# Optimization experiments

Measured on AMD Instinct MI355X. Metric: run time of the kernel, lower is better.

The kernel has to match this reference:

```python
import jax, jax.numpy as jnp
import numpy as np

N_DATA = 131072
N_HID = 32768
D = 256
E1 = 524288  # data -> hidden
E2 = 524288  # hidden -> hidden
E3 = 524288  # hidden -> data


def setup_inputs() -> dict:
    key = jax.random.key(0)
    ks = jax.random.split(key, 32)
    rn = lambda k, shape, s=0.05: (jax.random.normal(k, shape, jnp.float32) * s)
    inp = {
        "data_x": jax.random.normal(ks[0], (N_DATA, 8), jnp.float32),
        "hidden_x": jax.random.normal(ks[1], (N_HID, 3), jnp.float32),
        "dh_src": jax.random.randint(ks[2], (E1,), 0, N_DATA, jnp.int32),
        "dh_dst": jax.random.randint(ks[3], (E1,), 0, N_HID, jnp.int32),
        "hh_src": jax.random.randint(ks[4], (E2,), 0, N_HID, jnp.int32),
        "hh_dst": jax.random.randint(ks[5], (E2,), 0, N_HID, jnp.int32),
        "hd_src": jax.random.randint(ks[6], (E3,), 0, N_HID, jnp.int32),
        "hd_dst": jax.random.randint(ks[7], (E3,), 0, N_DATA, jnp.int32),
        # encoder params
        "enc_src_w": rn(ks[8], (D, 8)), "enc_src_b": rn(ks[9], (D,)),
        "enc_dst_w": rn(ks[10], (D, 3)), "enc_dst_b": rn(ks[11], (D,)),
        "enc_wl": rn(ks[12], (D, D)), "enc_bl": rn(ks[13], (D,)), "enc_wr": rn(ks[14], (D, D)),
        # processor params
        "proc_wl": rn(ks[15], (D, D)), "proc_bl": rn(ks[16], (D,)), "proc_wr": rn(ks[17], (D, D)),
        "proc_mlp_w": rn(ks[18], (D, D)), "proc_mlp_b": rn(ks[19], (D,)),
        # decoder params
        "dec_src_w": rn(ks[20], (D, D)), "dec_src_b": rn(ks[21], (D,)),
        "dec_dst_w": rn(ks[22], (D, 8)), "dec_dst_b": rn(ks[23], (D,)),
        "dec_wl": rn(ks[24], (D, D)), "dec_bl": rn(ks[25], (D,)), "dec_wr": rn(ks[26], (D, D)),
        "out_w": rn(ks[27], (8, D)), "out_b": rn(ks[28], (8,)),
    }
    return inp


def _gelu(x):
    return jax.nn.gelu(x, approximate=False)  # torch nn.GELU default (erf)


def _sage(x_src, x_dst, src, dst, wl, bl, wr, n_dst):
    """PyG SAGEConv, mean aggregation: lin_l(mean_j x_src[j]) + lin_r(x_dst)."""
    msg = x_src[src]                                              # [E, D] gather
    agg = jax.ops.segment_sum(msg, dst, num_segments=n_dst)       # [n_dst, D]
    cnt = jax.ops.segment_sum(jnp.ones((src.shape[0], 1), msg.dtype), dst,
                              num_segments=n_dst)
    mean = agg / jnp.maximum(cnt, 1.0)
    return mean @ wl.T + bl + x_dst @ wr.T


def reference(data_x, hidden_x, dh_src, dh_dst, hh_src, hh_dst, hd_src, hd_dst,
              enc_src_w, enc_src_b, enc_dst_w, enc_dst_b, enc_wl, enc_bl, enc_wr,
              proc_wl, proc_bl, proc_wr, proc_mlp_w, proc_mlp_b,
              dec_src_w, dec_src_b, dec_dst_w, dec_dst_b, dec_wl, dec_bl, dec_wr,
              out_w, out_b):
    # ---- encoder: data -> hidden ----
    h_data = _gelu(data_x @ enc_src_w.T + enc_src_b)
    h_hid = _gelu(hidden_x @ enc_dst_w.T + enc_dst_b)
    h_hid = _gelu(_sage(h_data, h_hid, dh_src, dh_dst, enc_wl, enc_bl, enc_wr, N_HID))
    # ---- processor: hidden -> hidden, then GELU-Linear-GELU MLP ----
    h_hid = _sage(h_hid, h_hid, hh_src, hh_dst, proc_wl, proc_bl, proc_wr, N_HID)
    h_hid = _gelu(_gelu(h_hid) @ proc_mlp_w.T + proc_mlp_b)
    # ---- decoder: hidden -> data ----
    s = _gelu(h_hid @ dec_src_w.T + dec_src_b)
    d = _gelu(data_x @ dec_dst_w.T + dec_dst_b)
    d = _gelu(_sage(s, d, hd_src, hd_dst, dec_wl, dec_bl, dec_wr, N_DATA))
    return d @ out_w.T + out_b  # [N_DATA, 8]
```

## Files before the change

kernel.cpp:

```cpp
#include <hip/hip_runtime.h>
#include <stdint.h>

#define NDATA 131072
#define NHID  32768
#define NEDGE 524288

typedef __bf16 bf16_t;
typedef __bf16 bf16x4 __attribute__((ext_vector_type(4)));
typedef __bf16 bf16x8 __attribute__((ext_vector_type(8)));
typedef float  f32x4  __attribute__((ext_vector_type(4)));

__device__ __forceinline__ float gelu_f(float x) {
    return 0.5f * x * (1.0f + erff(x * 0.7071067811865476f));
}

__device__ __forceinline__ void glds16(const void* g, void* l) {
    auto* gp = reinterpret_cast<const __attribute__((address_space(1))) uint32_t*>(
        reinterpret_cast<uintptr_t>(g));
    auto* lp = reinterpret_cast<__attribute__((address_space(3))) uint32_t*>(
        reinterpret_cast<uintptr_t>(l));
    __builtin_amdgcn_global_load_lds(gp, lp, 16, 0, 0);
}

struct WPtrs { const float* p[9]; };

__global__ __launch_bounds__(256)
void cvt_w_kernel(WPtrs wp, bf16_t* __restrict__ out) {
    const int i = blockIdx.x * 256 + threadIdx.x;
    if (i < 8 * 65536) {
        const int wsel = i >> 16, off = i & 65535;
        out[i] = (bf16_t)wp.p[wsel][off];
    } else {
        out[i] = (bf16_t)wp.p[8][i - 8 * 65536];
    }
}

struct EdgePtrs { const int* src[3]; const int* dst[3]; };

__device__ __forceinline__ int cnt_off_of(int g) { return g == 0 ? 0 : (g == 1 ? NHID : 2 * NHID); }
__device__ __forceinline__ int rp_off_of(int g)  { return g == 0 ? 0 : (g == 1 ? NHID + 1 : 2 * NHID + 2); }
__device__ __forceinline__ int shift_of(int g)   { return g == 2 ? 10 : 8; }

__global__ __launch_bounds__(256)
void hist3(EdgePtrs ep, int* __restrict__ cnt_all) {
    const int g = blockIdx.x >> 11;
    const int i = ((blockIdx.x & 2047) << 8) + threadIdx.x;
    atomicAdd(&cnt_all[cnt_off_of(g) + ep.dst[g][i]], 1);
}

__global__ __launch_bounds__(256)
void scan_blk3(const int* __restrict__ cnt_all, int* __restrict__ pre_all,
               int* __restrict__ blk) {
    __shared__ int sh[256];
    const int bid = blockIdx.x;
    int g, local;
    if (bid < 32)      { g = 0; local = bid; }
    else if (bid < 64) { g = 1; local = bid - 32; }
    else               { g = 2; local = bid - 64; }
    const int t = threadIdx.x;
    const int cbase = cnt_off_of(g) + local * 1024 + t * 4;
    const int pbase = rp_off_of(g)  + local * 1024 + t * 4;
    int4 v = *(const int4*)(cnt_all + cbase);
    sh[t] = v.x + v.y + v.z + v.w;
    __syncthreads();
    for (int off = 1; off < 256; off <<= 1) {
        int other = 0;
        if (t >= off) other = sh[t - off];
        __syncthreads();
        if (t >= off) sh[t] += other;
        __syncthreads();
    }
    const int excl = (t == 0) ? 0 : sh[t - 1];
    int4 o;
    o.x = excl; o.y = o.x + v.x; o.z = o.y + v.y; o.w = o.z + v.z;
    *(int4*)(pre_all + pbase) = o;
    if (t == 255) blk[bid] = sh[255];
}

__global__ __launch_bounds__(256)
void scan_add3(const int* __restrict__ pre_all, const int* __restrict__ blk,
               int* __restrict__ rp_all, int* __restrict__ binA) {
    __shared__ int sh[256];
    const int bid = blockIdx.x;
    int g, local, gbase;
    if (bid < 32)      { g = 0; local = bid;      gbase = 0; }
    else if (bid < 64) { g = 1; local = bid - 32; gbase = 32; }
    else               { g = 2; local = bid - 64; gbase = 64; }
    const int t = threadIdx.x;
    int part = 0;
    if (t < local) part = blk[gbase + t];
    sh[t] = part;
    __syncthreads();
    for (int o2 = 128; o2 > 0; o2 >>= 1) {
        if (t < o2) sh[t] += sh[t + o2];
        __syncthreads();
    }
    const int off = sh[0];
    const int idx = local * 1024 + t * 4;
    const int pbase = rp_off_of(g) + idx;
    int4 v = *(const int4*)(pre_all + pbase);
    v.x += off; v.y += off; v.z += off; v.w += off;
    *(int4*)(rp_all + pbase) = v;
    const int bw = 1 << shift_of(g);
    if ((idx & (bw - 1)) == 0) binA[g * 128 + (idx >> shift_of(g))] = v.x;
    if (local == 0 && t == 0) {
        const int n = (g == 2) ? NDATA : NHID;
        rp_all[rp_off_of(g) + n] = NEDGE;
    }
}

__global__ __launch_bounds__(256)
void partition3(EdgePtrs ep, int* __restrict__ binA, int2* __restrict__ pairs) {
    __shared__ int hist[128], base[128], cur[128];
    const int g = blockIdx.x >> 7;
    const int blk = blockIdx.x & 127;
    const int t = threadIdx.x;
    const int shift = shift_of(g);
    const int e_base = blk * 4096;
    const int* src = ep.src[g];
    const int* dst = ep.dst[g];
    if (t < 128) { hist[t] = 0; cur[t] = 0; }
    __syncthreads();
    #pragma unroll
    for (int it = 0; it < 16; ++it) {
        const int d = dst[e_base + it * 256 + t];
        atomicAdd(&hist[d >> shift], 1);
    }
    __syncthreads();
    if (t < 128) base[t] = atomicAdd(&binA[g * 128 + t], hist[t]);
    __syncthreads();
    #pragma unroll
    for (int it = 0; it < 16; ++it) {
        const int e = e_base + it * 256 + t;
        const int s = src[e], d = dst[e];
        const int b = d >> shift;
        const int l = atomicAdd(&cur[b], 1);
        pairs[(size_t)g * NEDGE + base[b] + l] = make_int2(s, d);
    }
}

__global__ __launch_bounds__(256)
void binsort3(const int2* __restrict__ pairs, const int* __restrict__ rp_all,
              int* __restrict__ sorted_all) {
    __shared__ int cur[1024];
    const int g = blockIdx.x >> 7;
    const int b = blockIdx.x & 127;
    const int t = threadIdx.x;
    const int shift = shift_of(g);
    const int W = 1 << shift;
    const int d0 = b << shift;
    const int rpo = rp_off_of(g);
    for (int i = t; i < W; i += 256) cur[i] = rp_all[rpo + d0 + i];
    __syncthreads();
    const int e0 = rp_all[rpo + d0];
    const int e1 = rp_all[rpo + d0 + W];
    for (int e = e0 + t; e < e1; e += 256) {
        const int2 p = pairs[(size_t)g * NEDGE + e];
        const int pos = atomicAdd(&cur[p.y - d0], 1);
        sorted_all[(size_t)g * NEDGE + pos] = p.x;
    }
}

__global__ __launch_bounds__(256)
void csr_gather_mean(const bf16_t* __restrict__ feat, const int* __restrict__ row_ptr,
                     const int* __restrict__ sorted_src, bf16_t* __restrict__ mean, int n) {
    const int lane = threadIdx.x & 63;
    const int half = lane >> 5;
    const int col8 = (lane & 31) * 8;
    const int w = blockIdx.x * 4 + (threadIdx.x >> 6);
    if (w >= n) return;
    const int e0 = row_ptr[w], e1 = row_ptr[w + 1];
    float acc[8] = {0.f, 0.f, 0.f, 0.f, 0.f, 0.f, 0.f, 0.f};
    int e = e0 + half;
    for (; e + 2 < e1; e += 4) {
        const int s0 = sorted_src[e], s1 = sorted_src[e + 2];
        const bf16x8 v0 = *(const bf16x8*)(feat + (size_t)s0 * 256 + col8);
        const bf16x8 v1 = *(const bf16x8*)(feat + (size_t)s1 * 256 + col8);
        #pragma unroll
        for (int j = 0; j < 8; ++j) acc[j] += (float)v0[j] + (float)v1[j];
    }
    for (; e < e1; e += 2) {
        const int s0 = sorted_src[e];
        const bf16x8 v0 = *(const bf16x8*)(feat + (size_t)s0 * 256 + col8);
        #pragma unroll
        for (int j = 0; j < 8; ++j) acc[j] += (float)v0[j];
    }
    #pragma unroll
    for (int j = 0; j < 8; ++j) acc[j] += __shfl_xor(acc[j], 32, 64);
    if (half == 0) {
        const float ic = 1.0f / fmaxf((float)(e1 - e0), 1.0f);
        bf16x8 r;
        #pragma unroll
        for (int j = 0; j < 8; ++j) r[j] = (bf16_t)(acc[j] * ic);
        *(bf16x8*)(mean + (size_t)w * 256 + col8) = r;
    }
}

__global__ __launch_bounds__(256)
void enc_both(const float* __restrict__ hx, const float* __restrict__ w3,
              const float* __restrict__ b3, bf16_t* __restrict__ out3,
              const float* __restrict__ dx, const float* __restrict__ w8,
              const float* __restrict__ b8, bf16_t* __restrict__ out8) {
    __shared__ float ws[8 * 256];
    __shared__ float bs[256];
    const int t = threadIdx.x;
    const bool is8 = (blockIdx.x >= 512);
    if (is8) {
        #pragma unroll
        for (int j = 0; j < 8; ++j) ws[j * 256 + t] = w8[t * 8 + j];
        bs[t] = b8[t];
    } else {
        #pragma unroll
        for (int j = 0; j < 3; ++j) ws[j * 256 + t] = w3[t * 3 + j];
        bs[t] = b3[t];
    }
    __syncthreads();
    const int lane = t & 63, wv = t >> 6;
    const int f0 = lane * 4;
    const float4 b4 = *(const float4*)(&bs[f0]);
    if (!is8) {
        for (int node = blockIdx.x * 4 + wv; node < NHID; node += 512 * 4) {
            const float* xr = hx + (size_t)node * 3;
            float xv[3];
            #pragma unroll
            for (int j = 0; j < 3; ++j) xv[j] = xr[j];
            float a0 = b4.x, a1 = b4.y, a2 = b4.z, a3 = b4.w;
            #pragma unroll
            for (int j = 0; j < 3; ++j) {
                const float4 w4 = *(const float4*)(&ws[j * 256 + f0]);
                a0 += xv[j] * w4.x; a1 += xv[j] * w4.y;
                a2 += xv[j] * w4.z; a3 += xv[j] * w4.w;
            }
            bf16x4 r;
            r[0] = (bf16_t)gelu_f(a0); r[1] = (bf16_t)gelu_f(a1);
            r[2] = (bf16_t)gelu_f(a2); r[3] = (bf16_t)gelu_f(a3);
            *(bf16x4*)(out3 + (size_t)node * 256 + f0) = r;
        }
    } else {
        for (int node = (blockIdx.x - 512) * 4 + wv; node < NDATA; node += 2048 * 4) {
            const float* xr = dx + (size_t)node * 8;
            float xv[8];
            #pragma unroll
            for (int j = 0; j < 8; ++j) xv[j] = xr[j];
            float a0 = b4.x, a1 = b4.y, a2 = b4.z, a3 = b4.w;
            #pragma unroll
            for (int j = 0; j < 8; ++j) {
                const float4 w4 = *(const float4*)(&ws[j * 256 + f0]);
                a0 += xv[j] * w4.x; a1 += xv[j] * w4.y;
                a2 += xv[j] * w4.z; a3 += xv[j] * w4.w;
            }
            bf16x4 r;
            r[0] = (bf16_t)gelu_f(a0); r[1] = (bf16_t)gelu_f(a1);
            r[2] = (bf16_t)gelu_f(a2); r[3] = (bf16_t)gelu_f(a3);
            *(bf16x4*)(out8 + (size_t)node * 256 + f0) = r;
        }
    }
}

template<int DUAL>
__global__ __launch_bounds__(256)
void mfma_gemm(const bf16_t* __restrict__ A1, const bf16_t* __restrict__ W1,
               const bf16_t* __restrict__ A2, const bf16_t* __restrict__ W2,
               const float* __restrict__ bias, bf16_t* __restrict__ C) {
    __shared__ bf16_t As[4 * 64 * 8];
    __shared__ bf16_t Bs[4 * 128 * 8];
    const int t = threadIdx.x;
    const int w = t >> 6, lane = t & 63;
    const int l15 = lane & 15, l4 = lane >> 4;
    const int m0 = (blockIdx.x >> 1) * 64;
    const int n0 = (blockIdx.x & 1) * 128;

    f32x4 acc[4][2];
    #pragma unroll
    for (int nb = 0; nb < 2; ++nb) {
        const float bv = bias[n0 + w * 32 + nb * 16 + l15];
        #pragma unroll
        for (int m = 0; m < 4; ++m) {
            acc[m][nb][0] = bv; acc[m][nb][1] = bv; acc[m][nb][2] = bv; acc[m][nb][3] = bv;
        }
    }

    #pragma unroll
    for (int p = 0; p <= DUAL; ++p) {
        const bf16_t* Ap = p ? A2 : A1;
        const bf16_t* Wp = p ? W2 : W1;
        for (int kt = 0; kt < 8; ++kt) {
            const int k0 = kt * 32;
            __syncthreads();
            glds16(Ap + (size_t)(m0 + lane) * 256 + k0 + w * 8, &As[(w * 64) * 8]);
            glds16(Wp + (size_t)(n0 + lane) * 256 + k0 + w * 8, &Bs[(w * 128) * 8]);
            glds16(Wp + (size_t)(n0 + 64 + lane) * 256 + k0 + w * 8, &Bs[(w * 128 + 64) * 8]);
            __syncthreads();
            bf16x8 af[4], bfr[2];
            #pragma unroll
            for (int m = 0; m < 4; ++m)
                af[m] = *(const bf16x8*)(&As[(l4 * 64 + m * 16 + l15) * 8]);
            #pragma unroll
            for (int nb = 0; nb < 2; ++nb)
                bfr[nb] = *(const bf16x8*)(&Bs[(l4 * 128 + w * 32 + nb * 16 + l15) * 8]);
            #pragma unroll
            for (int m = 0; m < 4; ++m)
                #pragma unroll
                for (int nb = 0; nb < 2; ++nb)
                    acc[m][nb] = __builtin_amdgcn_mfma_f32_16x16x32_bf16(af[m], bfr[nb], acc[m][nb], 0, 0, 0);
        }
    }

    #pragma unroll
    for (int m = 0; m < 4; ++m) {
        #pragma unroll
        for (int nb = 0; nb < 2; ++nb) {
            const int col = n0 + w * 32 + nb * 16 + l15;
            #pragma unroll
            for (int i = 0; i < 4; ++i) {
                const int row = m0 + m * 16 + l4 * 4 + i;
                C[(size_t)row * 256 + col] = (bf16_t)gelu_f(acc[m][nb][i]);
            }
        }
    }
}

__global__ __launch_bounds__(256)
void dec_gemm(const bf16_t* __restrict__ A1, const bf16_t* __restrict__ W1,
              const float* __restrict__ xdat, const float* __restrict__ Wd,
              const float* __restrict__ bd, const bf16_t* __restrict__ W2,
              const float* __restrict__ bias, const bf16_t* __restrict__ owb,
              const float* __restrict__ ob, float* __restrict__ out) {
    __shared__ __align__(16) char smem[25600];
    bf16_t* As   = (bf16_t*)smem;
    bf16_t* Bs   = (bf16_t*)(smem + 4096);
    bf16_t* wd16 = (bf16_t*)(smem + 20480);
    float*  bdS  = (float*)(smem + 24576);
    bf16_t* tt   = (bf16_t*)smem;
    float*  part = (float*)(smem + 16384);

    const int t = threadIdx.x;
    const int w = t >> 6, lane = t & 63;
    const int l15 = lane & 15, l4 = lane >> 4;
    const int m0 = blockIdx.x * 64;

    {
        const float4 wa = *(const float4*)(Wd + t * 8);
        const float4 wb = *(const float4*)(Wd + t * 8 + 4);
        bf16x8 wv;
        wv[0] = (bf16_t)wa.x; wv[1] = (bf16_t)wa.y; wv[2] = (bf16_t)wa.z; wv[3] = (bf16_t)wa.w;
        wv[4] = (bf16_t)wb.x; wv[5] = (bf16_t)wb.y; wv[6] = (bf16_t)wb.z; wv[7] = (bf16_t)wb.w;
        *(bf16x8*)(&wd16[t * 8]) = wv;
        bdS[t] = bd[t];
    }
    bf16x8 af_x;
    #pragma unroll
    for (int j = 0; j < 8; ++j) af_x[j] = (bf16_t)0.0f;
    if (l4 == 0) {
        const float* xrp = xdat + (size_t)(m0 + w * 16 + l15) * 8;
        const float4 xa = *(const float4*)(xrp);
        const float4 xb = *(const float4*)(xrp + 4);
        af_x[0] = (bf16_t)xa.x; af_x[1] = (bf16_t)xa.y; af_x[2] = (bf16_t)xa.z; af_x[3] = (bf16_t)xa.w;
        af_x[4] = (bf16_t)xb.x; af_x[5] = (bf16_t)xb.y; af_x[6] = (bf16_t)xb.z; af_x[7] = (bf16_t)xb.w;
    }

    f32x4 acc[4][4];
    #pragma unroll
    for (int nb = 0; nb < 4; ++nb) {
        const float bv = bias[w * 64 + nb * 16 + l15];
        #pragma unroll
        for (int m = 0; m < 4; ++m) {
            acc[m][nb][0] = bv; acc[m][nb][1] = bv; acc[m][nb][2] = bv; acc[m][nb][3] = bv;
        }
    }
    __syncthreads();

    #pragma unroll
    for (int p = 0; p < 2; ++p) {
        const bf16_t* Wp = p ? W2 : W1;
        for (int kt = 0; kt < 8; ++kt) {
            const int k0 = kt * 32;
            __syncthreads();
            if (p == 0) {
                glds16(A1 + (size_t)(m0 + lane) * 256 + k0 + w * 8, &As[(w * 64) * 8]);
            } else {
                #pragma unroll
                for (int nb2 = 0; nb2 < 2; ++nb2) {
                    const int cl = nb2 * 16 + l15;
                    const int col = k0 + cl;
                    f32x4 ad;
                    const float bv = bdS[col];
                    ad[0] = bv; ad[1] = bv; ad[2] = bv; ad[3] = bv;
                    bf16x8 bf_d;
                    #pragma unroll
                    for (int j = 0; j < 8; ++j) bf_d[j] = (bf16_t)0.0f;
                    if (l4 == 0) bf_d = *(const bf16x8*)(&wd16[col * 8]);
                    ad = __builtin_amdgcn_mfma_f32_16x16x32_bf16(af_x, bf_d, ad, 0, 0, 0);
                    const int kq = cl >> 3, jj = cl & 7;
                    #pragma unroll
                    for (int i = 0; i < 4; ++i)
                        As[(kq * 64 + w * 16 + l4 * 4 + i) * 8 + jj] = (bf16_t)gelu_f(ad[i]);
                }
            }
            #pragma unroll
            for (int q = 0; q < 4; ++q)
                glds16(Wp + (size_t)(w * 64 + lane) * 256 + k0 + q * 8,
                       &Bs[(q * 256 + w * 64) * 8]);
            __syncthreads();
            bf16x8 af[4], bfr[4];
            #pragma unroll
            for (int m = 0; m < 4; ++m)
                af[m] = *(const bf16x8*)(&As[(l4 * 64 + m * 16 + l15) * 8]);
            #pragma unroll
            for (int nb = 0; nb < 4; ++nb)
                bfr[nb] = *(const bf16x8*)(&Bs[(l4 * 256 + w * 64 + nb * 16 + l15) * 8]);
            #pragma unroll
            for (int m = 0; m < 4; ++m)
                #pragma unroll
                for (int nb = 0; nb < 4; ++nb)
                    acc[m][nb] = __builtin_amdgcn_mfma_f32_16x16x32_bf16(af[m], bfr[nb], acc[m][nb], 0, 0, 0);
        }
    }

    __syncthreads();

    bf16x8 owf[2];
    #pragma unroll
    for (int s = 0; s < 2; ++s) {
        #pragma unroll
        for (int j = 0; j < 8; ++j) owf[s][j] = (bf16_t)0.0f;
        if (l15 < 8)
            owf[s] = *(const bf16x8*)(owb + l15 * 256 + w * 64 + s * 32 + l4 * 8);
    }

    bf16_t* ttw = tt + w * 2048;
    #pragma unroll
    for (int h = 0; h < 2; ++h) {
        #pragma unroll
        for (int mm = 0; mm < 2; ++mm) {
            const int m = h * 2 + mm;
            #pragma unroll
            for (int nb = 0; nb < 4; ++nb) {
                const int col = nb * 16 + l15;
                const int kg = col >> 3, cj = col & 7;
                #pragma unroll
                for (int i = 0; i < 4; ++i) {
                    const int rl = mm * 16 + l4 * 4 + i;
                    ttw[(kg * 32 + rl) * 8 + cj] = (bf16_t)gelu_f(acc[m][nb][i]);
                }
            }
        }
        f32x4 accp[2];
        #pragma unroll
        for (int mb = 0; mb < 2; ++mb) {
            accp[mb][0] = 0.f; accp[mb][1] = 0.f; accp[mb][2] = 0.f; accp[mb][3] = 0.f;
            #pragma unroll
            for (int s = 0; s < 2; ++s) {
                const bf16x8 af = *(const bf16x8*)(&ttw[((s * 4 + l4) * 32 + mb * 16 + l15) * 8]);
                accp[mb] = __builtin_amdgcn_mfma_f32_16x16x32_bf16(af, owf[s], accp[mb], 0, 0, 0);
            }
        }
        __syncthreads();
        #pragma unroll
        for (int mb = 0; mb < 2; ++mb)
            #pragma unroll
            for (int i = 0; i < 4; ++i)
                part[(w * 32 + mb * 16 + l4 * 4 + i) * 16 + l15] = accp[mb][i];
        __syncthreads();
        {
            const int row = t >> 3, o = t & 7;
            const float v = part[(0 * 32 + row) * 16 + o] + part[(1 * 32 + row) * 16 + o]
                          + part[(2 * 32 + row) * 16 + o] + part[(3 * 32 + row) * 16 + o] + ob[o];
            out[(size_t)(m0 + h * 32 + row) * 8 + o] = v;
        }
    }
}


extern "C" void kernel_launch(void* const* d_in, const int* in_sizes, int n_in,
                              void* d_out, int out_size, void* d_ws, size_t ws_size,
                              hipStream_t stream) {
    const float* data_x   = (const float*)d_in[0];
    const float* hidden_x = (const float*)d_in[1];
    const int* dh_src = (const int*)d_in[2];
    const int* dh_dst = (const int*)d_in[3];
    const int* hh_src = (const int*)d_in[4];
    const int* hh_dst = (const int*)d_in[5];
    const int* hd_src = (const int*)d_in[6];
    const int* hd_dst = (const int*)d_in[7];
    const float* enc_src_w = (const float*)d_in[8];
    const float* enc_src_b = (const float*)d_in[9];
    const float* enc_dst_w = (const float*)d_in[10];
    const float* enc_dst_b = (const float*)d_in[11];
    const float* enc_wl = (const float*)d_in[12];
    const float* enc_bl = (const float*)d_in[13];
    const float* enc_wr = (const float*)d_in[14];
    const float* proc_wl = (const float*)d_in[15];
    const float* proc_bl = (const float*)d_in[16];
    const float* proc_wr = (const float*)d_in[17];
    const float* proc_mlp_w = (const float*)d_in[18];
    const float* proc_mlp_b = (const float*)d_in[19];
    const float* dec_src_w = (const float*)d_in[20];
    const float* dec_src_b = (const float*)d_in[21];
    const float* dec_dst_w = (const float*)d_in[22];
    const float* dec_dst_b = (const float*)d_in[23];
    const float* dec_wl = (const float*)d_in[24];
    const float* dec_bl = (const float*)d_in[25];
    const float* dec_wr = (const float*)d_in[26];
    const float* out_w  = (const float*)d_in[27];
    const float* out_b  = (const float*)d_in[28];
    float* out = (float*)d_out;

    bf16_t* h_a   = (bf16_t*)d_ws;
    bf16_t* h_b   = h_a + (size_t)NHID * 256;
    bf16_t* h_c   = h_b + (size_t)NHID * 256;
    bf16_t* h_msg = h_c + (size_t)NHID * 256;
    bf16_t* dmean = h_msg + (size_t)NDATA * 256;
    bf16_t* wbuf  = dmean + (size_t)NDATA * 256;
    int* cnt_all    = (int*)(wbuf + 8 * 65536 + 2048);
    int* rp_all     = cnt_all + (2 * NHID + NDATA);
    int* sorted_all = rp_all + (2 * NHID + NDATA + 3);
    int* blk_sums   = sorted_all + (size_t)3 * NEDGE;
    int* binA       = blk_sums + 192;
    int2* pairs     = (int2*)(((uintptr_t)(binA + 384) + 15) & ~(uintptr_t)15);

    bf16_t* W_enc_wl  = wbuf + 0 * 65536;
    bf16_t* W_enc_wr  = wbuf + 1 * 65536;
    bf16_t* W_proc_wl = wbuf + 2 * 65536;
    bf16_t* W_proc_wr = wbuf + 3 * 65536;
    bf16_t* W_mlp     = wbuf + 4 * 65536;
    bf16_t* W_dec_src = wbuf + 5 * 65536;
    bf16_t* W_dec_wl  = wbuf + 6 * 65536;
    bf16_t* W_dec_wr  = wbuf + 7 * 65536;
    bf16_t* W_out     = wbuf + 8 * 65536;

    const int* rp_dh = rp_all;
    const int* rp_hh = rp_all + NHID + 1;
    const int* rp_hd = rp_all + 2 * NHID + 2;
    const int* so_dh = sorted_all;
    const int* so_hh = sorted_all + NEDGE;
    const int* so_hd = sorted_all + 2 * (size_t)NEDGE;

    WPtrs wp;
    wp.p[0] = enc_wl;  wp.p[1] = enc_wr;  wp.p[2] = proc_wl; wp.p[3] = proc_wr;
    wp.p[4] = proc_mlp_w; wp.p[5] = dec_src_w; wp.p[6] = dec_wl; wp.p[7] = dec_wr;
    wp.p[8] = out_w;
    cvt_w_kernel<<<2056, 256, 0, stream>>>(wp, wbuf);

    EdgePtrs ep;
    ep.src[0] = dh_src; ep.dst[0] = dh_dst;
    ep.src[1] = hh_src; ep.dst[1] = hh_dst;
    ep.src[2] = hd_src; ep.dst[2] = hd_dst;
    hipMemsetAsync(cnt_all, 0, (size_t)(2 * NHID + NDATA) * sizeof(int), stream);
    hist3<<<3 * 2048, 256, 0, stream>>>(ep, cnt_all);
    scan_blk3<<<192, 256, 0, stream>>>(cnt_all, rp_all, blk_sums);
    scan_add3<<<192, 256, 0, stream>>>(rp_all, blk_sums, rp_all, binA);
    partition3<<<3 * 128, 256, 0, stream>>>(ep, binA, pairs);
    binsort3<<<3 * 128, 256, 0, stream>>>(pairs, rp_all, sorted_all);

    enc_both<<<2560, 256, 0, stream>>>(hidden_x, enc_dst_w, enc_dst_b, h_a,
                                       data_x, enc_src_w, enc_src_b, h_msg);
    csr_gather_mean<<<NHID / 4, 256, 0, stream>>>(h_msg, rp_dh, so_dh, h_b, NHID);
    mfma_gemm<1><<<(NHID / 64) * 2, 256, 0, stream>>>(h_b, W_enc_wl, h_a, W_enc_wr, enc_bl, h_c);

    csr_gather_mean<<<NHID / 4, 256, 0, stream>>>(h_c, rp_hh, so_hh, h_a, NHID);
    mfma_gemm<1><<<(NHID / 64) * 2, 256, 0, stream>>>(h_a, W_proc_wl, h_c, W_proc_wr, proc_bl, h_b);
    mfma_gemm<0><<<(NHID / 64) * 2, 256, 0, stream>>>(h_b, W_mlp, nullptr, nullptr, proc_mlp_b, h_a);
    mfma_gemm<0><<<(NHID / 64) * 2, 256, 0, stream>>>(h_a, W_dec_src, nullptr, nullptr, dec_src_b, h_b);

    csr_gather_mean<<<NDATA / 4, 256, 0, stream>>>(h_b, rp_hd, so_hd, dmean, NDATA);
    dec_gemm<<<NDATA / 64, 256, 0, stream>>>(dmean, W_dec_wl, data_x, dec_dst_w, dec_dst_b,
                                             W_dec_wr, dec_bl, W_out, out_b, out);
}
```

Baseline: 466.1 us.

## Fuse CSR gather-mean into SAGE GEMM kernels via LDS-resident mean tiles

Removes the standalone csr_gather_mean launches. Each GEMM block now gathers and averages the neighbor features for its 64 rows directly into shared memory, then runs the lin_l MFMA pass from LDS and the lin_r pass with A read directly from global memory. This drops the write and re-read of the mean buffers, which matters most for the large decoder buffer, and saves three launches. In exchange, blocks become 64x256 tiles with much larger LDS footprints, halving the grid for the hidden-node GEMMs. The latency-bound gather may then run with lower occupancy, and each wave serializes its 16 rows.

```diff
diff --git a/kernel.cpp b/kernel.cpp
--- a/kernel.cpp
+++ b/kernel.cpp
@@ -20,6 +20,11 @@
     auto* lp = reinterpret_cast<__attribute__((address_space(3))) uint32_t*>(
         reinterpret_cast<uintptr_t>(l));
     __builtin_amdgcn_global_load_lds(gp, lp, 16, 0, 0);
+}
+
+__device__ __forceinline__ void vm_fence0() {
+    asm volatile("s_waitcnt vmcnt(0)" ::: "memory");
+    __builtin_amdgcn_sched_barrier(0);
 }
 
 struct WPtrs { const float* p[9]; };
@@ -162,41 +167,6 @@
 }
 
 __global__ __launch_bounds__(256)
-void csr_gather_mean(const bf16_t* __restrict__ feat, const int* __restrict__ row_ptr,
-                     const int* __restrict__ sorted_src, bf16_t* __restrict__ mean, int n) {
-    const int lane = threadIdx.x & 63;
-    const int half = lane >> 5;
-    const int col8 = (lane & 31) * 8;
-    const int w = blockIdx.x * 4 + (threadIdx.x >> 6);
-    if (w >= n) return;
-    const int e0 = row_ptr[w], e1 = row_ptr[w + 1];
-    float acc[8] = {0.f, 0.f, 0.f, 0.f, 0.f, 0.f, 0.f, 0.f};
-    int e = e0 + half;
-    for (; e + 2 < e1; e += 4) {
-        const int s0 = sorted_src[e], s1 = sorted_src[e + 2];
-        const bf16x8 v0 = *(const bf16x8*)(feat + (size_t)s0 * 256 + col8);
-        const bf16x8 v1 = *(const bf16x8*)(feat + (size_t)s1 * 256 + col8);
-        #pragma unroll
-        for (int j = 0; j < 8; ++j) acc[j] += (float)v0[j] + (float)v1[j];
-    }
-    for (; e < e1; e += 2) {
-        const int s0 = sorted_src[e];
-        const bf16x8 v0 = *(const bf16x8*)(feat + (size_t)s0 * 256 + col8);
-        #pragma unroll
-        for (int j = 0; j < 8; ++j) acc[j] += (float)v0[j];
-    }
-    #pragma unroll
-    for (int j = 0; j < 8; ++j) acc[j] += __shfl_xor(acc[j], 32, 64);
-    if (half == 0) {
-        const float ic = 1.0f / fmaxf((float)(e1 - e0), 1.0f);
-        bf16x8 r;
-        #pragma unroll
-        for (int j = 0; j < 8; ++j) r[j] = (bf16_t)(acc[j] * ic);
-        *(bf16x8*)(mean + (size_t)w * 256 + col8) = r;
-    }
-}
-
-__global__ __launch_bounds__(256)
 void enc_both(const float* __restrict__ hx, const float* __restrict__ w3,
               const float* __restrict__ b3, bf16_t* __restrict__ out3,
               const float* __restrict__ dx, const float* __restrict__ w8,
@@ -257,11 +227,128 @@
     }
 }
 
-template<int DUAL>
-__global__ __launch_bounds__(256)
-void mfma_gemm(const bf16_t* __restrict__ A1, const bf16_t* __restrict__ W1,
-               const bf16_t* __restrict__ A2, const bf16_t* __restrict__ W2,
-               const float* __restrict__ bias, bf16_t* __restrict__ C) {
+__device__ __forceinline__ void gather_tile(const bf16_t* __restrict__ feat,
+                                            const int* __restrict__ rp,
+                                            const int* __restrict__ ss,
+                                            bf16_t* __restrict__ Asg,
+                                            int m0, int w, int lane) {
+    const int half = lane >> 5;
+    const int kq = lane & 31;
+    const int colb = kq * 8;
+    for (int rr = 0; rr < 16; ++rr) {
+        const int row = w * 16 + rr;
+        const int g0 = rp[m0 + row], g1 = rp[m0 + row + 1];
+        float a8[8] = {0.f, 0.f, 0.f, 0.f, 0.f, 0.f, 0.f, 0.f};
+        int e = g0 + half;
+        for (; e + 2 < g1; e += 4) {
+            const int s0 = ss[e], s1 = ss[e + 2];
+            const bf16x8 v0 = *(const bf16x8*)(feat + (size_t)s0 * 256 + colb);
+            const bf16x8 v1 = *(const bf16x8*)(feat + (size_t)s1 * 256 + colb);
+            #pragma unroll
+            for (int j = 0; j < 8; ++j) a8[j] += (float)v0[j] + (float)v1[j];
+        }
+        for (; e < g1; e += 2) {
+            const int s0 = ss[e];
+            const bf16x8 v0 = *(const bf16x8*)(feat + (size_t)s0 * 256 + colb);
+            #pragma unroll
+            for (int j = 0; j < 8; ++j) a8[j] += (float)v0[j];
+        }
+        #pragma unroll
+        for (int j = 0; j < 8; ++j) a8[j] += __shfl_xor(a8[j], 32, 64);
+        if (half == 0) {
+            const float ic = 1.0f / fmaxf((float)(g1 - g0), 1.0f);
+            bf16x8 r;
+            #pragma unroll
+            for (int j = 0; j < 8; ++j) r[j] = (bf16_t)(a8[j] * ic);
+            *(bf16x8*)(&Asg[(kq * 64 + row) * 8]) = r;
+        }
+    }
+}
+
+__global__ __launch_bounds__(256)
+void gemm_gather(const bf16_t* __restrict__ feat, const int* __restrict__ rp,
+                 const int* __restrict__ ss, const bf16_t* __restrict__ W1,
+                 const bf16_t* __restrict__ A2, const bf16_t* __restrict__ W2,
+                 const float* __restrict__ bias, bf16_t* __restrict__ C) {
+    __shared__ bf16_t Asg[32 * 64 * 8];
+    __shared__ bf16_t Bs[4 * 256 * 8];
+    const int t = threadIdx.x;
+    const int w = t >> 6, lane = t & 63;
+    const int l15 = lane & 15, l4 = lane >> 4;
+    const int m0 = blockIdx.x * 64;
+
+    gather_tile(feat, rp, ss, Asg, m0, w, lane);
+
+    f32x4 acc[4][4];
+    #pragma unroll
+    for (int nb = 0; nb < 4; ++nb) {
+        const float bv = bias[w * 64 + nb * 16 + l15];
+        #pragma unroll
+        for (int m = 0; m < 4; ++m) {
+            acc[m][nb][0] = bv; acc[m][nb][1] = bv; acc[m][nb][2] = bv; acc[m][nb][3] = bv;
+        }
+    }
+    __syncthreads();
+
+    for (int kt = 0; kt < 8; ++kt) {
+        const int k0 = kt * 32;
+        #pragma unroll
+        for (int q = 0; q < 4; ++q)
+            glds16(W1 + (size_t)(w * 64 + lane) * 256 + k0 + q * 8,
+                   &Bs[(q * 256 + w * 64) * 8]);
+        vm_fence0();
+        bf16x8 af[4], bfr[4];
+        #pragma unroll
+        for (int m = 0; m < 4; ++m)
+            af[m] = *(const bf16x8*)(&Asg[((kt * 4 + l4) * 64 + m * 16 + l15) * 8]);
+        #pragma unroll
+        for (int nb = 0; nb < 4; ++nb)
+            bfr[nb] = *(const bf16x8*)(&Bs[(l4 * 256 + w * 64 + nb * 16 + l15) * 8]);
+        #pragma unroll
+        for (int m = 0; m < 4; ++m)
+            #pragma unroll
+            for (int nb = 0; nb < 4; ++nb)
+                acc[m][nb] = __builtin_amdgcn_mfma_f32_16x16x32_bf16(af[m], bfr[nb], acc[m][nb], 0, 0, 0);
+    }
+    for (int kt = 0; kt < 8; ++kt) {
+        const int k0 = kt * 32;
+        #pragma unroll
+        for (int q = 0; q < 4; ++q)
+            glds16(W2 + (size_t)(w * 64 + lane) * 256 + k0 + q * 8,
+                   &Bs[(q * 256 + w * 64) * 8]);
+        bf16x8 af[4];
+        #pragma unroll
+        for (int m = 0; m < 4; ++m)
+            af[m] = *(const bf16x8*)(A2 + (size_t)(m0 + m * 16 + l15) * 256 + k0 + l4 * 8);
+        vm_fence0();
+        bf16x8 bfr[4];
+        #pragma unroll
+        for (int nb = 0; nb < 4; ++nb)
+            bfr[nb] = *(const bf16x8*)(&Bs[(l4 * 256 + w * 64 + nb * 16 + l15) * 8]);
+        #pragma unroll
+        for (int m = 0; m < 4; ++m)
+            #pragma unroll
+            for (int nb = 0; nb < 4; ++nb)
+                acc[m][nb] = __builtin_amdgcn_mfma_f32_16x16x32_bf16(af[m], bfr[nb], acc[m][nb], 0, 0, 0);
+    }
+
+    #pragma unroll
+    for (int m = 0; m < 4; ++m) {
+        #pragma unroll
+        for (int nb = 0; nb < 4; ++nb) {
+            const int col = w * 64 + nb * 16 + l15;
+            #pragma unroll
+            for (int i = 0; i < 4; ++i) {
+                const int row = m0 + m * 16 + l4 * 4 + i;
+                C[(size_t)row * 256 + col] = (bf16_t)gelu_f(acc[m][nb][i]);
+            }
+        }
+    }
+}
+
+__global__ __launch_bounds__(256)
+void mfma_gemm0(const bf16_t* __restrict__ A1, const bf16_t* __restrict__ W1,
+                const float* __restrict__ bias, bf16_t* __restrict__ C) {
     __shared__ bf16_t As[4 * 64 * 8];
     __shared__ bf16_t Bs[4 * 128 * 8];
     const int t = threadIdx.x;
@@ -280,30 +367,25 @@
         }
     }
 
-    #pragma unroll
-    for (int p = 0; p <= DUAL; ++p) {
-        const bf16_t* Ap = p ? A2 : A1;
-        const bf16_t* Wp = p ? W2 : W1;
-        for (int kt = 0; kt < 8; ++kt) {
-            const int k0 = kt * 32;
-            __syncthreads();
-            glds16(Ap + (size_t)(m0 + lane) * 256 + k0 + w * 8, &As[(w * 64) * 8]);
-            glds16(Wp + (size_t)(n0 + lane) * 256 + k0 + w * 8, &Bs[(w * 128) * 8]);
-            glds16(Wp + (size_t)(n0 + 64 + lane) * 256 + k0 + w * 8, &Bs[(w * 128 + 64) * 8]);
-            __syncthreads();
-            bf16x8 af[4], bfr[2];
-            #pragma unroll
-            for (int m = 0; m < 4; ++m)
-                af[m] = *(const bf16x8*)(&As[(l4 * 64 + m * 16 + l15) * 8]);
+    for (int kt = 0; kt < 8; ++kt) {
+        const int k0 = kt * 32;
+        __syncthreads();
+        glds16(A1 + (size_t)(m0 + lane) * 256 + k0 + w * 8, &As[(w * 64) * 8]);
+        glds16(W1 + (size_t)(n0 + lane) * 256 + k0 + w * 8, &Bs[(w * 128) * 8]);
+        glds16(W1 + (size_t)(n0 + 64 + lane) * 256 + k0 + w * 8, &Bs[(w * 128 + 64) * 8]);
+        __syncthreads();
+        bf16x8 af[4], bfr[2];
+        #pragma unroll
+        for (int m = 0; m < 4; ++m)
+            af[m] = *(const bf16x8*)(&As[(l4 * 64 + m * 16 + l15) * 8]);
+        #pragma unroll
+        for (int nb = 0; nb < 2; ++nb)
+            bfr[nb] = *(const bf16x8*)(&Bs[(l4 * 128 + w * 32 + nb * 16 + l15) * 8]);
+        #pragma unroll
+        for (int m = 0; m < 4; ++m)
             #pragma unroll
             for (int nb = 0; nb < 2; ++nb)
-                bfr[nb] = *(const bf16x8*)(&Bs[(l4 * 128 + w * 32 + nb * 16 + l15) * 8]);
-            #pragma unroll
-            for (int m = 0; m < 4; ++m)
-                #pragma unroll
-                for (int nb = 0; nb < 2; ++nb)
-                    acc[m][nb] = __builtin_amdgcn_mfma_f32_16x16x32_bf16(af[m], bfr[nb], acc[m][nb], 0, 0, 0);
-        }
+                acc[m][nb] = __builtin_amdgcn_mfma_f32_16x16x32_bf16(af[m], bfr[nb], acc[m][nb], 0, 0, 0);
     }
 
     #pragma unroll
@@ -321,16 +403,17 @@
 }
 
 __global__ __launch_bounds__(256)
-void dec_gemm(const bf16_t* __restrict__ A1, const bf16_t* __restrict__ W1,
-              const float* __restrict__ xdat, const float* __restrict__ Wd,
-              const float* __restrict__ bd, const bf16_t* __restrict__ W2,
-              const float* __restrict__ bias, const bf16_t* __restrict__ owb,
-              const float* __restrict__ ob, float* __restrict__ out) {
-    __shared__ __align__(16) char smem[25600];
-    bf16_t* As   = (bf16_t*)smem;
-    bf16_t* Bs   = (bf16_t*)(smem + 4096);
-    bf16_t* wd16 = (bf16_t*)(smem + 20480);
-    float*  bdS  = (float*)(smem + 24576);
+void dec_gemm_g(const bf16_t* __restrict__ feat, const int* __restrict__ rp,
+                const int* __restrict__ ss, const bf16_t* __restrict__ W1,
+                const float* __restrict__ xdat, const float* __restrict__ Wd,
+                const float* __restrict__ bd, const bf16_t* __restrict__ W2,
+                const float* __restrict__ bias, const bf16_t* __restrict__ owb,
+                const float* __restrict__ ob, float* __restrict__ out) {
+    __shared__ __align__(16) char smem[57344];
+    bf16_t* Asg  = (bf16_t*)smem;
+    bf16_t* Bs   = (bf16_t*)(smem + 32768);
+    bf16_t* Asd  = (bf16_t*)(smem + 49152);
+    bf16_t* wd16 = (bf16_t*)(smem + 53248);
     bf16_t* tt   = (bf16_t*)smem;
     float*  part = (float*)(smem + 16384);
 
@@ -346,7 +429,6 @@
         wv[0] = (bf16_t)wa.x; wv[1] = (bf16_t)wa.y; wv[2] = (bf16_t)wa.z; wv[3] = (bf16_t)wa.w;
         wv[4] = (bf16_t)wb.x; wv[5] = (bf16_t)wb.y; wv[6] = (bf16_t)wb.z; wv[7] = (bf16_t)wb.w;
         *(bf16x8*)(&wd16[t * 8]) = wv;
-        bdS[t] = bd[t];
     }
     bf16x8 af_x;
     #pragma unroll
@@ -359,6 +441,8 @@
         af_x[4] = (bf16_t)xb.x; af_x[5] = (bf16_t)xb.y; af_x[6] = (bf16_t)xb.z; af_x[7] = (bf16_t)xb.w;
     }
 
+    gather_tile(feat, rp, ss, Asg, m0, w, lane);
+
     f32x4 acc[4][4];
     #pragma unroll
     for (int nb = 0; nb < 4; ++nb) {
@@ -370,51 +454,63 @@
     }
     __syncthreads();
 
-    #pragma unroll
-    for (int p = 0; p < 2; ++p) {
-        const bf16_t* Wp = p ? W2 : W1;
-        for (int kt = 0; kt < 8; ++kt) {
-            const int k0 = kt * 32;
-            __syncthreads();
-            if (p == 0) {
-                glds16(A1 + (size_t)(m0 + lane) * 256 + k0 + w * 8, &As[(w * 64) * 8]);
-            } else {
-                #pragma unroll
-                for (int nb2 = 0; nb2 < 2; ++nb2) {
-                    const int cl = nb2 * 16 + l15;
-                    const int col = k0 + cl;
-                    f32x4 ad;
-                    const float bv = bdS[col];
-                    ad[0] = bv; ad[1] = bv; ad[2] = bv; ad[3] = bv;
-                    bf16x8 bf_d;
-                    #pragma unroll
-                    for (int j = 0; j < 8; ++j) bf_d[j] = (bf16_t)0.0f;
-                    if (l4 == 0) bf_d = *(const bf16x8*)(&wd16[col * 8]);
-                    ad = __builtin_amdgcn_mfma_f32_16x16x32_bf16(af_x, bf_d, ad, 0, 0, 0);
-                    const int kq = cl >> 3, jj = cl & 7;
-                    #pragma unroll
-                    for (int i = 0; i < 4; ++i)
-                        As[(kq * 64 + w * 16 + l4 * 4 + i) * 8 + jj] = (bf16_t)gelu_f(ad[i]);
-                }
-            }
-            #pragma unroll
-            for (int q = 0; q < 4; ++q)
-                glds16(Wp + (size_t)(w * 64 + lane) * 256 + k0 + q * 8,
-                       &Bs[(q * 256 + w * 64) * 8]);
-            __syncthreads();
-            bf16x8 af[4], bfr[4];
-            #pragma unroll
-            for (int m = 0; m < 4; ++m)
-                af[m] = *(const bf16x8*)(&As[(l4 * 64 + m * 16 + l15) * 8]);
+    for (int kt = 0; kt < 8; ++kt) {
+        const int k0 = kt * 32;
+        #pragma unroll
+        for (int q = 0; q < 4; ++q)
+            glds16(W1 + (size_t)(w * 64 + lane) * 256 + k0 + q * 8,
+                   &Bs[(q * 256 + w * 64) * 8]);
+        vm_fence0();
+        bf16x8 af[4], bfr[4];
+        #pragma unroll
+        for (int m = 0; m < 4; ++m)
+            af[m] = *(const bf16x8*)(&Asg[((kt * 4 + l4) * 64 + m * 16 + l15) * 8]);
+        #pragma unroll
+        for (int nb = 0; nb < 4; ++nb)
+            bfr[nb] = *(const bf16x8*)(&Bs[(l4 * 256 + w * 64 + nb * 16 + l15) * 8]);
+        #pragma unroll
+        for (int m = 0; m < 4; ++m)
             #pragma unroll
             for (int nb = 0; nb < 4; ++nb)
-                bfr[nb] = *(const bf16x8*)(&Bs[(l4 * 256 + w * 64 + nb * 16 + l15) * 8]);
-            #pragma unroll
-            for (int m = 0; m < 4; ++m)
-                #pragma unroll
-                for (int nb = 0; nb < 4; ++nb)
-                    acc[m][nb] = __builtin_amdgcn_mfma_f32_16x16x32_bf16(af[m], bfr[nb], acc[m][nb], 0, 0, 0);
-        }
+                acc[m][nb] = __builtin_amdgcn_mfma_f32_16x16x32_bf16(af[m], bfr[nb], acc[m][nb], 0, 0, 0);
+    }
+    for (int kt = 0; kt < 8; ++kt) {
+        const int k0 = kt * 32;
+        __syncthreads();
+        #pragma unroll
+        for (int nb2 = 0; nb2 < 2; ++nb2) {
+            const int cl = nb2 * 16 + l15;
+            const int col = k0 + cl;
+            f32x4 ad;
+            const float bv = bd[col];
+            ad[0] = bv; ad[1] = bv; ad[2] = bv; ad[3] = bv;
+            bf16x8 bf_d;
+            #pragma unroll
+            for (int j = 0; j < 8; ++j) bf_d[j] = (bf16_t)0.0f;
+            if (l4 == 0) bf_d = *(const bf16x8*)(&wd16[col * 8]);
+            ad = __builtin_amdgcn_mfma_f32_16x16x32_bf16(af_x, bf_d, ad, 0, 0, 0);
+            const int kq = cl >> 3, jj = cl & 7;
+            #pragma unroll
+            for (int i = 0; i < 4; ++i)
+                Asd[(kq * 64 + w * 16 + l4 * 4 + i) * 8 + jj] = (bf16_t)gelu_f(ad[i]);
+        }
+        #pragma unroll
+        for (int q = 0; q < 4; ++q)
+            glds16(W2 + (size_t)(w * 64 + lane) * 256 + k0 + q * 8,
+                   &Bs[(q * 256 + w * 64) * 8]);
+        __syncthreads();
+        bf16x8 af[4], bfr[4];
+        #pragma unroll
+        for (int m = 0; m < 4; ++m)
+            af[m] = *(const bf16x8*)(&Asd[(l4 * 64 + m * 16 + l15) * 8]);
+        #pragma unroll
+        for (int nb = 0; nb < 4; ++nb)
+            bfr[nb] = *(const bf16x8*)(&Bs[(l4 * 256 + w * 64 + nb * 16 + l15) * 8]);
+        #pragma unroll
+        for (int m = 0; m < 4; ++m)
+            #pragma unroll
+            for (int nb = 0; nb < 4; ++nb)
+                acc[m][nb] = __builtin_amdgcn_mfma_f32_16x16x32_bf16(af[m], bfr[nb], acc[m][nb], 0, 0, 0);
     }
 
     __syncthreads();
@@ -510,8 +606,7 @@
     bf16_t* h_b   = h_a + (size_t)NHID * 256;
     bf16_t* h_c   = h_b + (size_t)NHID * 256;
     bf16_t* h_msg = h_c + (size_t)NHID * 256;
-    bf16_t* dmean = h_msg + (size_t)NDATA * 256;
-    bf16_t* wbuf  = dmean + (size_t)NDATA * 256;
+    bf16_t* wbuf  = h_msg + (size_t)NDATA * 256;
     int* cnt_all    = (int*)(wbuf + 8 * 65536 + 2048);
     int* rp_all     = cnt_all + (2 * NHID + NDATA);
     int* sorted_all = rp_all + (2 * NHID + NDATA + 3);
@@ -555,15 +650,16 @@
 
     enc_both<<<2560, 256, 0, stream>>>(hidden_x, enc_dst_w, enc_dst_b, h_a,
                                        data_x, enc_src_w, enc_src_b, h_msg);
-    csr_gather_mean<<<NHID / 4, 256, 0, stream>>>(h_msg, rp_dh, so_dh, h_b, NHID);
-    mfma_gemm<1><<<(NHID / 64) * 2, 256, 0, stream>>>(h_b, W_enc_wl, h_a, W_enc_wr, enc_bl, h_c);
-
-    csr_gather_mean<<<NHID / 4, 256, 0, stream>>>(h_c, rp_hh, so_hh, h_a, NHID);
-    mfma_gemm<1><<<(NHID / 64) * 2, 256, 0, stream>>>(h_a, W_proc_wl, h_c, W_proc_wr, proc_bl, h_b);
-    mfma_gemm<0><<<(NHID / 64) * 2, 256, 0, stream>>>(h_b, W_mlp, nullptr, nullptr, proc_mlp_b, h_a);
-    mfma_gemm<0><<<(NHID / 64) * 2, 256, 0, stream>>>(h_a, W_dec_src, nullptr, nullptr, dec_src_b, h_b);
-
-    csr_gather_mean<<<NDATA / 4, 256, 0, stream>>>(h_b, rp_hd, so_hd, dmean, NDATA);
-    dec_gemm<<<NDATA / 64, 256, 0, stream>>>(dmean, W_dec_wl, data_x, dec_dst_w, dec_dst_b,
-                                             W_dec_wr, dec_bl, W_out, out_b, out);
-}
+
+    gemm_gather<<<NHID / 64, 256, 0, stream>>>(h_msg, rp_dh, so_dh, W_enc_wl,
+                                               h_a, W_enc_wr, enc_bl, h_b);
+
+    gemm_gather<<<NHID / 64, 256, 0, stream>>>(h_b, rp_hh, so_hh, W_proc_wl,
+                                               h_b, W_proc_wr, proc_bl, h_c);
+    mfma_gemm0<<<(NHID / 64) * 2, 256, 0, stream>>>(h_c, W_mlp, proc_mlp_b, h_a);
+    mfma_gemm0<<<(NHID / 64) * 2, 256, 0, stream>>>(h_a, W_dec_src, dec_src_b, h_b);
+
+    dec_gemm_g<<<NDATA / 64, 256, 0, stream>>>(h_b, rp_hd, so_hd, W_dec_wl,
+                                               data_x, dec_dst_w, dec_dst_b,
+                                               W_dec_wr, dec_bl, W_out, out_b, out);
+}
```

Result: slower. 598.7 us (+28.5%).

## Apply decoder lin_l before aggregation on hidden nodes; unroll gather by four

Applied to the files above, without the earlier changes.

Uses linearity of the mean to move the decoder lin_l projection ahead of aggregation. It now runs as a plain GEMM on the 32768 hidden nodes instead of the 131072 data nodes, and the projected mean is added as the initial accumulator in the decoder GEMM. This removes one K=256 GEMM pass over the large data set. The extra cost is another bf16 round trip, since the intermediate is rounded before aggregation. The gather loop is also unrolled to four edges per half-wave for more memory-level parallelism.

```diff
diff --git a/kernel.cpp b/kernel.cpp
--- a/kernel.cpp
+++ b/kernel.cpp
@@ -172,12 +172,16 @@
     const int e0 = row_ptr[w], e1 = row_ptr[w + 1];
     float acc[8] = {0.f, 0.f, 0.f, 0.f, 0.f, 0.f, 0.f, 0.f};
     int e = e0 + half;
-    for (; e + 2 < e1; e += 4) {
-        const int s0 = sorted_src[e], s1 = sorted_src[e + 2];
+    for (; e + 6 < e1; e += 8) {
+        const int s0 = sorted_src[e],     s1 = sorted_src[e + 2];
+        const int s2 = sorted_src[e + 4], s3 = sorted_src[e + 6];
         const bf16x8 v0 = *(const bf16x8*)(feat + (size_t)s0 * 256 + col8);
         const bf16x8 v1 = *(const bf16x8*)(feat + (size_t)s1 * 256 + col8);
-        #pragma unroll
-        for (int j = 0; j < 8; ++j) acc[j] += (float)v0[j] + (float)v1[j];
+        const bf16x8 v2 = *(const bf16x8*)(feat + (size_t)s2 * 256 + col8);
+        const bf16x8 v3 = *(const bf16x8*)(feat + (size_t)s3 * 256 + col8);
+        #pragma unroll
+        for (int j = 0; j < 8; ++j)
+            acc[j] += ((float)v0[j] + (float)v1[j]) + ((float)v2[j] + (float)v3[j]);
     }
     for (; e < e1; e += 2) {
         const int s0 = sorted_src[e];
@@ -257,7 +261,7 @@
     }
 }
 
-template<int DUAL>
+template<int DUAL, int ACT>
 __global__ __launch_bounds__(256)
 void mfma_gemm(const bf16_t* __restrict__ A1, const bf16_t* __restrict__ W1,
                const bf16_t* __restrict__ A2, const bf16_t* __restrict__ W2,
@@ -273,7 +277,7 @@
     f32x4 acc[4][2];
     #pragma unroll
     for (int nb = 0; nb < 2; ++nb) {
-        const float bv = bias[n0 + w * 32 + nb * 16 + l15];
+        const float bv = bias ? bias[n0 + w * 32 + nb * 16 + l15] : 0.0f;
         #pragma unroll
         for (int m = 0; m < 4; ++m) {
             acc[m][nb][0] = bv; acc[m][nb][1] = bv; acc[m][nb][2] = bv; acc[m][nb][3] = bv;
@@ -314,18 +318,19 @@
             #pragma unroll
             for (int i = 0; i < 4; ++i) {
                 const int row = m0 + m * 16 + l4 * 4 + i;
-                C[(size_t)row * 256 + col] = (bf16_t)gelu_f(acc[m][nb][i]);
+                const float v = acc[m][nb][i];
+                C[(size_t)row * 256 + col] = (bf16_t)(ACT ? gelu_f(v) : v);
             }
         }
     }
 }
 
 __global__ __launch_bounds__(256)
-void dec_gemm(const bf16_t* __restrict__ A1, const bf16_t* __restrict__ W1,
-              const float* __restrict__ xdat, const float* __restrict__ Wd,
-              const float* __restrict__ bd, const bf16_t* __restrict__ W2,
-              const float* __restrict__ bias, const bf16_t* __restrict__ owb,
-              const float* __restrict__ ob, float* __restrict__ out) {
+void dec_gemm_m(const bf16_t* __restrict__ A1mean,
+                const float* __restrict__ xdat, const float* __restrict__ Wd,
+                const float* __restrict__ bd, const bf16_t* __restrict__ W2,
+                const float* __restrict__ bias, const bf16_t* __restrict__ owb,
+                const float* __restrict__ ob, float* __restrict__ out) {
     __shared__ __align__(16) char smem[25600];
     bf16_t* As   = (bf16_t*)smem;
     bf16_t* Bs   = (bf16_t*)(smem + 4096);
@@ -362,59 +367,56 @@
     f32x4 acc[4][4];
     #pragma unroll
     for (int nb = 0; nb < 4; ++nb) {
-        const float bv = bias[w * 64 + nb * 16 + l15];
+        const int col = w * 64 + nb * 16 + l15;
+        const float bv = bias[col];
         #pragma unroll
         for (int m = 0; m < 4; ++m) {
-            acc[m][nb][0] = bv; acc[m][nb][1] = bv; acc[m][nb][2] = bv; acc[m][nb][3] = bv;
-        }
-    }
-    __syncthreads();
-
-    #pragma unroll
-    for (int p = 0; p < 2; ++p) {
-        const bf16_t* Wp = p ? W2 : W1;
-        for (int kt = 0; kt < 8; ++kt) {
-            const int k0 = kt * 32;
-            __syncthreads();
-            if (p == 0) {
-                glds16(A1 + (size_t)(m0 + lane) * 256 + k0 + w * 8, &As[(w * 64) * 8]);
-            } else {
-                #pragma unroll
-                for (int nb2 = 0; nb2 < 2; ++nb2) {
-                    const int cl = nb2 * 16 + l15;
-                    const int col = k0 + cl;
-                    f32x4 ad;
-                    const float bv = bdS[col];
-                    ad[0] = bv; ad[1] = bv; ad[2] = bv; ad[3] = bv;
-                    bf16x8 bf_d;
-                    #pragma unroll
-                    for (int j = 0; j < 8; ++j) bf_d[j] = (bf16_t)0.0f;
-                    if (l4 == 0) bf_d = *(const bf16x8*)(&wd16[col * 8]);
-                    ad = __builtin_amdgcn_mfma_f32_16x16x32_bf16(af_x, bf_d, ad, 0, 0, 0);
-                    const int kq = cl >> 3, jj = cl & 7;
-                    #pragma unroll
-                    for (int i = 0; i < 4; ++i)
-                        As[(kq * 64 + w * 16 + l4 * 4 + i) * 8 + jj] = (bf16_t)gelu_f(ad[i]);
-                }
+            #pragma unroll
+            for (int i = 0; i < 4; ++i) {
+                const int row = m0 + m * 16 + l4 * 4 + i;
+                acc[m][nb][i] = bv + (float)A1mean[(size_t)row * 256 + col];
             }
-            #pragma unroll
-            for (int q = 0; q < 4; ++q)
-                glds16(Wp + (size_t)(w * 64 + lane) * 256 + k0 + q * 8,
-                       &Bs[(q * 256 + w * 64) * 8]);
-            __syncthreads();
-            bf16x8 af[4], bfr[4];
-            #pragma unroll
-            for (int m = 0; m < 4; ++m)
-                af[m] = *(const bf16x8*)(&As[(l4 * 64 + m * 16 + l15) * 8]);
+        }
+    }
+    __syncthreads();
+
+    for (int kt = 0; kt < 8; ++kt) {
+        const int k0 = kt * 32;
+        __syncthreads();
+        #pragma unroll
+        for (int nb2 = 0; nb2 < 2; ++nb2) {
+            const int cl = nb2 * 16 + l15;
+            const int col = k0 + cl;
+            f32x4 ad;
+            const float bv = bdS[col];
+            ad[0] = bv; ad[1] = bv; ad[2] = bv; ad[3] = bv;
+            bf16x8 bf_d;
+            #pragma unroll
+            for (int j = 0; j < 8; ++j) bf_d[j] = (bf16_t)0.0f;
+            if (l4 == 0) bf_d = *(const bf16x8*)(&wd16[col * 8]);
+            ad = __builtin_amdgcn_mfma_f32_16x16x32_bf16(af_x, bf_d, ad, 0, 0, 0);
+            const int kq = cl >> 3, jj = cl & 7;
+            #pragma unroll
+            for (int i = 0; i < 4; ++i)
+                As[(kq * 64 + w * 16 + l4 * 4 + i) * 8 + jj] = (bf16_t)gelu_f(ad[i]);
+        }
+        #pragma unroll
+        for (int q = 0; q < 4; ++q)
+            glds16(W2 + (size_t)(w * 64 + lane) * 256 + k0 + q * 8,
+                   &Bs[(q * 256 + w * 64) * 8]);
+        __syncthreads();
+        bf16x8 af[4], bfr[4];
+        #pragma unroll
+        for (int m = 0; m < 4; ++m)
+            af[m] = *(const bf16x8*)(&As[(l4 * 64 + m * 16 + l15) * 8]);
+        #pragma unroll
+        for (int nb = 0; nb < 4; ++nb)
+            bfr[nb] = *(const bf16x8*)(&Bs[(l4 * 256 + w * 64 + nb * 16 + l15) * 8]);
+        #pragma unroll
+        for (int m = 0; m < 4; ++m)
             #pragma unroll
             for (int nb = 0; nb < 4; ++nb)
-                bfr[nb] = *(const bf16x8*)(&Bs[(l4 * 256 + w * 64 + nb * 16 + l15) * 8]);
-            #pragma unroll
-            for (int m = 0; m < 4; ++m)
-                #pragma unroll
-                for (int nb = 0; nb < 4; ++nb)
-                    acc[m][nb] = __builtin_amdgcn_mfma_f32_16x16x32_bf16(af[m], bfr[nb], acc[m][nb], 0, 0, 0);
-        }
+                acc[m][nb] = __builtin_amdgcn_mfma_f32_16x16x32_bf16(af[m], bfr[nb], acc[m][nb], 0, 0, 0);
     }
 
     __syncthreads();
@@ -556,14 +558,15 @@
     enc_both<<<2560, 256, 0, stream>>>(hidden_x, enc_dst_w, enc_dst_b, h_a,
                                        data_x, enc_src_w, enc_src_b, h_msg);
     csr_gather_mean<<<NHID / 4, 256, 0, stream>>>(h_msg, rp_dh, so_dh, h_b, NHID);
-    mfma_gemm<1><<<(NHID / 64) * 2, 256, 0, stream>>>(h_b, W_enc_wl, h_a, W_enc_wr, enc_bl, h_c);
+    mfma_gemm<1, 1><<<(NHID / 64) * 2, 256, 0, stream>>>(h_b, W_enc_wl, h_a, W_enc_wr, enc_bl, h_c);
 
     csr_gather_mean<<<NHID / 4, 256, 0, stream>>>(h_c, rp_hh, so_hh, h_a, NHID);
-    mfma_gemm<1><<<(NHID / 64) * 2, 256, 0, stream>>>(h_a, W_proc_wl, h_c, W_proc_wr, proc_bl, h_b);
-    mfma_gemm<0><<<(NHID / 64) * 2, 256, 0, stream>>>(h_b, W_mlp, nullptr, nullptr, proc_mlp_b, h_a);
-    mfma_gemm<0><<<(NHID / 64) * 2, 256, 0, stream>>>(h_a, W_dec_src, nullptr, nullptr, dec_src_b, h_b);
-
-    csr_gather_mean<<<NDATA / 4, 256, 0, stream>>>(h_b, rp_hd, so_hd, dmean, NDATA);
-    dec_gemm<<<NDATA / 64, 256, 0, stream>>>(dmean, W_dec_wl, data_x, dec_dst_w, dec_dst_b,
-                                             W_dec_wr, dec_bl, W_out, out_b, out);
-}
+    mfma_gemm<1, 1><<<(NHID / 64) * 2, 256, 0, stream>>>(h_a, W_proc_wl, h_c, W_proc_wr, proc_bl, h_b);
+    mfma_gemm<0, 1><<<(NHID / 64) * 2, 256, 0, stream>>>(h_b, W_mlp, nullptr, nullptr, proc_mlp_b, h_a);
+    mfma_gemm<0, 1><<<(NHID / 64) * 2, 256, 0, stream>>>(h_a, W_dec_src, nullptr, nullptr, dec_src_b, h_b);
+
+    mfma_gemm<0, 0><<<(NHID / 64) * 2, 256, 0, stream>>>(h_b, W_dec_wl, nullptr, nullptr, nullptr, h_c);
+    csr_gather_mean<<<NDATA / 4, 256, 0, stream>>>(h_c, rp_hd, so_hd, dmean, NDATA);
+    dec_gemm_m<<<NDATA / 64, 256, 0, stream>>>(dmean, data_x, dec_dst_w, dec_dst_b,
+                                               W_dec_wr, dec_bl, W_out, out_b, out);
+}
```

Result: no change. 461.6 us (-1.0%).
